# Kernel optimization log

Hardware: AMD Instinct MI355X
Metric: run time of the kernel (lower is better)

## Reference

```python
import jax, jax.numpy as jnp
import numpy as np

K_QUERY = 3    # opt.k: each point assigned to its 3 nearest SOM nodes
SOM_K = 9      # opt.som_k: 3x3 SOM neighborhood
EPS = 1e-5


def _lin1d(w, b, h):
    # 1x1 conv1d + relu: h is B,Cin,N
    return jax.nn.relu(jnp.einsum('oi,bin->bon', w, h) + b[None, :, None])


def _lin2d(w, b, h):
    # 1x1 conv2d + relu: h is B,Cin,M,K
    return jax.nn.relu(jnp.einsum('oi,bimk->bomk', w, h) + b[None, :, None, None])


def _gather_nb(feat, I):
    # feat: B,C,M ; I: B,M,K (node indices) -> B,C,M,K
    B, C, M = feat.shape
    K = I.shape[2]
    idx = jnp.broadcast_to(I[:, None, :, :], (B, C, M, K))
    return jnp.take_along_axis(feat[:, :, :, None], idx, axis=2)


def setup_inputs():
    key = jax.random.key(0)
    B, N, M = 8, 8192, 64
    ks = jax.random.split(key, 16)
    def w(k, o, i):
        return (jax.random.normal(k, (o, i), jnp.float32) / np.sqrt(i).astype(np.float32))
    return {
        'x': jax.random.normal(ks[0], (B, 3, N), jnp.float32),
        'sn': jax.random.normal(ks[1], (B, 3, N), jnp.float32),
        'node': jax.random.normal(ks[2], (B, 3, M), jnp.float32),
        'node_knn_I': jax.random.randint(ks[3], (B, M, SOM_K), 0, M),
        # PointResNet(6, [64,128,256,384])
        'pr_w0': w(ks[4], 64, 6), 'pr_b0': jnp.zeros((64,), jnp.float32),
        'pr_w1': w(ks[5], 128, 64), 'pr_b1': jnp.zeros((128,), jnp.float32),
        'pr_w2': w(ks[6], 256, 128), 'pr_b2': jnp.zeros((256,), jnp.float32),
        'pr_w3': w(ks[7], 384, 64 + 256), 'pr_b3': jnp.zeros((384,), jnp.float32),
        # KNNModule(3+384, (512,512))
        'knn_w0': w(ks[8], 512, 3 + 384), 'knn_b0': jnp.zeros((512,), jnp.float32),
        'knn_w1': w(ks[9], 512, 512), 'knn_b1': jnp.zeros((512,), jnp.float32),
        # final PointNet(3+512, (768,1024))
        'fin_w0': w(ks[10], 768, 3 + 512), 'fin_b0': jnp.zeros((768,), jnp.float32),
        'fin_w1': w(ks[11], 1024, 768), 'fin_b1': jnp.zeros((1024,), jnp.float32),
    }


def reference(x, sn, node, node_knn_I, pr_w0, pr_b0, pr_w1, pr_b1, pr_w2, pr_b2,
              pr_w3, pr_b3, knn_w0, knn_b0, knn_w1, knn_b1, fin_w0, fin_b0,
              fin_w1, fin_b1):
    B, _, N = x.shape
    M = node.shape[2]
    k = K_QUERY
    kN = k * N
    # --- som.query_topk: assign each point to its k nearest SOM nodes ---
    xd = jax.lax.stop_gradient(x)
    dist = jnp.sum((node[:, :, :, None] - xd[:, :, None, :]) ** 2, axis=1)  # B,M,N
    _, idx = jax.lax.top_k(-jnp.swapaxes(dist, 1, 2), k)                     # B,N,k
    min_idx = jnp.transpose(idx, (0, 2, 1)).reshape(B, kN)                   # B,kN (k blocks of N)
    mask = jax.nn.one_hot(min_idx, M, dtype=x.dtype)                         # B,kN,M
    mask_row_sum = jnp.sum(mask, axis=1)                                     # B,M
    mask_row_max = jnp.max(mask, axis=1) > 0                                 # B,M
    x_stack = jnp.tile(x, (1, 1, k))                                         # B,3,kN
    sn_stack = jnp.tile(sn, (1, 1, k))
    # --- masked segment-mean -> per-node cluster centers (detached) ---
    cluster_mean = jax.lax.stop_gradient(
        jnp.einsum('bcn,bnm->bcm', x_stack, mask) / (mask_row_sum[:, None, :] + EPS))
    centers = jnp.einsum('bcm,bnm->bcn', cluster_mean, mask)                 # B,3,kN
    x_decentered = jax.lax.stop_gradient(x_stack - centers)
    x_aug = jnp.concatenate([x_decentered, sn_stack], axis=1)                # B,6,kN
    # --- PointResNet(6,[64,128,256,384]) ---
    h0 = _lin1d(pr_w0, pr_b0, x_aug)
    h1 = _lin1d(pr_w1, pr_b1, h0)
    h2 = _lin1d(pr_w2, pr_b2, h1)
    first = _lin1d(pr_w3, pr_b3, jnp.concatenate([h0, h2], axis=1))          # B,384,kN
    # --- index_max scatter-max: per-node per-channel max over assigned points ---
    seg = (min_idx + (jnp.arange(B)[:, None] * M)).reshape(-1)               # (B*kN,)
    data = jnp.transpose(first, (0, 2, 1)).reshape(B * kN, -1)               # (B*kN, C)
    node_max = jax.ops.segment_max(data, seg, num_segments=B * M)            # (B*M, C)
    node_max = jnp.transpose(node_max.reshape(B, M, -1), (0, 2, 1))          # B,C,M
    # empty nodes gather index 0 in the original (gather_index * mask_row_max)
    first_masked_max = jnp.where(mask_row_max[:, None, :], node_max, first[:, :, 0:1])
    # --- KNNModule over SOM nodes (som_k=9, 'avg' centering) ---
    coord_knn = _gather_nb(cluster_mean, node_knn_I)                         # B,3,M,K
    center = jnp.mean(coord_knn, axis=3)                                     # B,3,M
    feat_knn = _gather_nb(first_masked_max, node_knn_I)                      # B,384,M,K
    aug = jnp.concatenate([coord_knn - center[:, :, :, None], feat_knn], axis=1)
    g = _lin2d(knn_w1, knn_b1, _lin2d(knn_w0, knn_b0, aug))                  # B,512,M,K
    knn_feature = jnp.max(g, axis=3)                                         # B,512,M
    # --- final PointNet(3+512,(768,1024)) + global max pool ---
    f = _lin1d(fin_w1, fin_b1,
               _lin1d(fin_w0, fin_b0, jnp.concatenate([center, knn_feature], axis=1)))
    return jnp.max(f, axis=2)                                                # B,1024
```

## Files before the change

kernel.cpp:

```cpp
#include <hip/hip_runtime.h>

typedef unsigned short u16;
typedef unsigned int   u32;
typedef _Float16 f16;
typedef _Float16 f16x8 __attribute__((ext_vector_type(8)));
typedef _Float16 f16x4 __attribute__((ext_vector_type(4)));
typedef float    f32x4 __attribute__((ext_vector_type(4)));

#define BQ 8
#define NQ 8192
#define MQ 64
#define SEGS (BQ*MQ)
#define MAXCHUNK 3584
#define KBA 10
#define NCOLS_D 4608

#define OFF_IDX      (size_t)0
#define OFF_PERM     (size_t)786432
#define OFF_CNT      (size_t)1572864
#define OFF_SUMS     (size_t)1574912
#define OFF_OFFS     (size_t)1581056
#define OFF_CURSOR   (size_t)1583360
#define OFF_NCHUNK   (size_t)1585408
#define OFF_CHUNKTAB (size_t)1585664
#define OFF_MEAN     (size_t)1614336
#define OFF_FALLBACK (size_t)1620480
#define OFF_NODEMAX  (size_t)1632768
#define OFF_CENTER   (size_t)2419200
#define OFF_W1P      (size_t)2425344
#define OFF_W2P      (size_t)2441728
#define OFF_W3P      (size_t)2507264
#define OFF_KNW0P    (size_t)2753024
#define OFF_KNW1P    (size_t)3179008
#define OFF_FINW0P   (size_t)3703296
#define OFF_FINW1P   (size_t)4538880
#define OFF_AUG      (size_t)6111744
#define OFF_MID1     (size_t)9945600
#define OFF_GBUF     (size_t)14664192
#define OFF_KEIN     (size_t)19382784
#define OFF_MIDE     (size_t)19939840

__device__ __forceinline__ void wpack(const float* __restrict__ W, f16* __restrict__ out,
                                      int K, int KB, int NF, int idx) {
  int e  = idx & 7;
  int l  = (idx >> 3) & 63;
  int kb = (idx >> 9) % KB;
  int rt = idx / (KB << 9);
  int row = rt * 16 + (l & 15);
  int c = kb * 32 + ((l >> 4) << 3) + e;
  int oc;
  if (NF < 0) oc = (c < K) ? c : -1;
  else        oc = (c < NF) ? (3 + c) : ((c < NF + 3) ? (c - NF) : -1);
  out[idx] = (oc >= 0) ? (f16)W[row * K + oc] : (f16)0.f;
}
__global__ __launch_bounds__(256) void kW(
    const float* pr_w1, const float* pr_w2, const float* pr_w3,
    const float* knn_w0, const float* knn_w1, const float* fin_w0, const float* fin_w1,
    f16* w1p, f16* w2p, f16* w3p, f16* knw0p, f16* knw1p, f16* finw0p, f16* finw1p) {
  int blk = blockIdx.x;
  int t = threadIdx.x;
  if (blk < 32)        wpack(pr_w1,  w1p,   64,  2, -1, blk * 256 + t);
  else if (blk < 160)  wpack(pr_w2,  w2p,  128,  4, -1, (blk - 32) * 256 + t);
  else if (blk < 640)  wpack(pr_w3,  w3p,  320, 10, -1, (blk - 160) * 256 + t);
  else if (blk < 1472) wpack(knn_w0, knw0p, 387, 13, 384, (blk - 640) * 256 + t);
  else if (blk < 2496) wpack(knn_w1, knw1p, 512, 16, -1, (blk - 1472) * 256 + t);
  else if (blk < 4128) wpack(fin_w0, finw0p, 515, 17, 512, (blk - 2496) * 256 + t);
  else                 wpack(fin_w1, finw1p, 768, 24, -1, (blk - 4128) * 256 + t);
}

__global__ __launch_bounds__(256) void kA(const float* __restrict__ x, const float* __restrict__ node,
                                          int* __restrict__ idx_buf, int* __restrict__ cnt,
                                          float* __restrict__ sums) {
#pragma clang fp contract(off)
  __shared__ float ns[3][64];
  __shared__ int cbin[64];
  __shared__ float sbin[3][64];
  int b = blockIdx.y;
  int t = threadIdx.x;
  if (t < 192) { int c = t >> 6, m = t & 63; ns[c][m] = node[(b * 3 + c) * 64 + m]; }
  if (t < 64) { cbin[t] = 0; sbin[0][t] = 0.f; sbin[1][t] = 0.f; sbin[2][t] = 0.f; }
  __syncthreads();
  int n = blockIdx.x * 256 + t;
  float x0 = x[(b * 3 + 0) * NQ + n];
  float x1 = x[(b * 3 + 1) * NQ + n];
  float x2 = x[(b * 3 + 2) * NQ + n];
  float d0 = 3.4e38f, d1 = 3.4e38f, d2 = 3.4e38f;
  int i0 = 0, i1 = 0, i2 = 0;
  for (int m = 0; m < 64; ++m) {
    float da = ns[0][m] - x0;
    float db = ns[1][m] - x1;
    float dc = ns[2][m] - x2;
    float d = da * da + db * db + dc * dc;
    if (d < d0)      { d2 = d1; i2 = i1; d1 = d0; i1 = i0; d0 = d; i0 = m; }
    else if (d < d1) { d2 = d1; i2 = i1; d1 = d;  i1 = m; }
    else if (d < d2) { d2 = d;  i2 = m; }
  }
  int base = (b * NQ + n) * 3;
  idx_buf[base + 0] = i0; idx_buf[base + 1] = i1; idx_buf[base + 2] = i2;
  int ms[3] = {i0, i1, i2};
  #pragma unroll
  for (int j = 0; j < 3; ++j) {
    int m = ms[j];
    atomicAdd(&cbin[m], 1);
    atomicAdd(&sbin[0][m], x0);
    atomicAdd(&sbin[1][m], x1);
    atomicAdd(&sbin[2][m], x2);
  }
  __syncthreads();
  if (t < 64 && cbin[t] > 0) {
    atomicAdd(&cnt[b * 64 + t], cbin[t]);
    atomicAdd(&sums[(b * 64 + t) * 3 + 0], sbin[0][t]);
    atomicAdd(&sums[(b * 64 + t) * 3 + 1], sbin[1][t]);
    atomicAdd(&sums[(b * 64 + t) * 3 + 2], sbin[2][t]);
  }
}

__global__ __launch_bounds__(256) void kB(const int* __restrict__ cnt, const float* __restrict__ sums,
                                          int* __restrict__ offs, int* __restrict__ cursor,
                                          int* __restrict__ nchunks, int* __restrict__ chunk_tab,
                                          float* __restrict__ mean) {
  __shared__ int sps[256], spc[256];
  int t = threadIdx.x;
  int c0 = cnt[2 * t], c1 = cnt[2 * t + 1];
  sps[t] = c0 + c1;
  spc[t] = ((c0 + 63) >> 6) + ((c1 + 63) >> 6);
  __syncthreads();
  for (int d = 1; d < 256; d <<= 1) {
    int a = 0, q = 0;
    if (t >= d) { a = sps[t - d]; q = spc[t - d]; }
    __syncthreads();
    if (t >= d) { sps[t] += a; spc[t] += q; }
    __syncthreads();
  }
  int pbase = t ? sps[t - 1] : 0;
  int cbase = t ? spc[t - 1] : 0;
  offs[2 * t] = pbase;        offs[2 * t + 1] = pbase + c0;
  cursor[2 * t] = pbase;      cursor[2 * t + 1] = pbase + c0;
  if (t == 255) { offs[512] = sps[255]; nchunks[0] = spc[255]; }
  int st = pbase, ci = cbase, s = 2 * t, c = c0;
  #pragma unroll
  for (int rep = 0; rep < 2; ++rep) {
    while (c > 0) {
      int l = c > 64 ? 64 : c;
      chunk_tab[2 * ci] = (s << 16) | l;
      chunk_tab[2 * ci + 1] = st;
      st += l; c -= l; ++ci;
    }
    s = 2 * t + 1; c = c1; st = pbase + c0;
  }
  for (int i = t; i < SEGS * 3; i += 256) mean[i] = sums[i] / ((float)cnt[i / 3] + 1e-5f);
}

__global__ __launch_bounds__(256) void kA2(const int* __restrict__ idx_buf, int* __restrict__ cursor,
                                           int* __restrict__ perm) {
  int b = blockIdx.y;
  int n = blockIdx.x * 256 + threadIdx.x;
  int base = (b * NQ + n) * 3;
  #pragma unroll
  for (int j = 0; j < 3; ++j) {
    int m = idx_buf[base + j];
    int pos = atomicAdd(&cursor[b * 64 + m], 1);
    perm[pos] = (b << 21) | (n << 8) | (j << 6) | m;
  }
}

__global__ __launch_bounds__(256) void kCtr(const float* __restrict__ mean,
                                            const int* __restrict__ knn_I,
                                            float* __restrict__ centerb) {
  int seg = blockIdx.x * 256 + threadIdx.x;
  if (seg >= SEGS) return;
  int b = seg >> 6;
  float s0 = 0, s1 = 0, s2 = 0;
  for (int kk = 0; kk < 9; ++kk) {
    int nb = knn_I[seg * 9 + kk];
    s0 += mean[(b * 64 + nb) * 3 + 0];
    s1 += mean[(b * 64 + nb) * 3 + 1];
    s2 += mean[(b * 64 + nb) * 3 + 2];
  }
  centerb[seg * 3 + 0] = s0 * (1.f / 9.f);
  centerb[seg * 3 + 1] = s1 * (1.f / 9.f);
  centerb[seg * 3 + 2] = s2 * (1.f / 9.f);
}

__global__ __launch_bounds__(512) void kC(
    const float* __restrict__ x, const float* __restrict__ sn,
    const float* __restrict__ mean, const int* __restrict__ perm,
    const int* __restrict__ chunk_tab, const int* __restrict__ nchunks,
    const float* __restrict__ w0, const float* __restrict__ b0v,
    const f16* __restrict__ w1p, const float* __restrict__ b1v,
    const f16* __restrict__ w2p, const float* __restrict__ b2v,
    const f16* __restrict__ w3p, const float* __restrict__ b3v,
    float* __restrict__ node_max, float* __restrict__ fallback) {
  __shared__ __align__(16) f16 bufA[4 * KBA * 64 * 8];
  __shared__ __align__(16) f16 bufH1[4 * 4 * 64 * 8];
  __shared__ float in_s[6][64];
  __shared__ int flag_s[64];
  int blk = blockIdx.x;
  if (blk >= nchunks[0]) return;
  int e0    = chunk_tab[2 * blk];
  int start = chunk_tab[2 * blk + 1];
  int seg = e0 >> 16, len = e0 & 0xffff;
  int b = seg >> 6;
  int tid = threadIdx.x;
  if (tid < 64) {
    float v0 = 0, v1 = 0, v2 = 0, v3 = 0, v4 = 0, v5 = 0;
    int fl = 0;
    if (tid < len) {
      int rec = perm[start + tid];
      int n = (rec >> 8) & 0x1fff;
      int j = (rec >> 6) & 3;
      const float* xb = x  + (size_t)b * 3 * NQ;
      const float* sb = sn + (size_t)b * 3 * NQ;
      v0 = xb[n]          - mean[seg * 3 + 0];
      v1 = xb[NQ + n]     - mean[seg * 3 + 1];
      v2 = xb[2 * NQ + n] - mean[seg * 3 + 2];
      v3 = sb[n]; v4 = sb[NQ + n]; v5 = sb[2 * NQ + n];
      fl = (n == 0 && j == 0) ? 1 : 0;
    }
    in_s[0][tid] = v0; in_s[1][tid] = v1; in_s[2][tid] = v2;
    in_s[3][tid] = v3; in_s[4][tid] = v4; in_s[5][tid] = v5;
    flag_s[tid] = fl;
  }
  __syncthreads();
  int wid  = __builtin_amdgcn_readfirstlane(tid >> 6);
  int lane = tid & 63;
  int pcol = lane & 15;
  int g    = lane >> 4;

  {
    float a0 = in_s[0][lane], a1 = in_s[1][lane], a2 = in_s[2][lane];
    float a3 = in_s[3][lane], a4 = in_s[4][lane], a5 = in_s[5][lane];
    f16x8 v;
    #pragma unroll
    for (int i = 0; i < 8; ++i) {
      const float* wr = w0 + (wid * 8 + i) * 6;
      float s = b0v[wid * 8 + i];
      s = fmaf(wr[0], a0, s); s = fmaf(wr[1], a1, s); s = fmaf(wr[2], a2, s);
      s = fmaf(wr[3], a3, s); s = fmaf(wr[4], a4, s); s = fmaf(wr[5], a5, s);
      v[i] = (f16)fmaxf(s, 0.f);
    }
    int kb = wid >> 2, q = wid & 3;
    *(f16x8*)&bufA[(((lane >> 4) * KBA + kb) * 64 + pcol + 16 * q) * 8] = v;
  }
  __syncthreads();

  f32x4 acc1[4] = {};
  #pragma unroll
  for (int kb = 0; kb < 2; ++kb) {
    f16x8 af = *(const f16x8*)(w1p + (size_t)((wid * 2 + kb) * 64 + lane) * 8);
    #pragma unroll
    for (int pt = 0; pt < 4; ++pt) {
      f16x8 bf = *(const f16x8*)&bufA[((pt * KBA + kb) * 64 + lane) * 8];
      acc1[pt] = __builtin_amdgcn_mfma_f32_16x16x32_f16(af, bf, acc1[pt], 0, 0, 0);
    }
  }
  {
    float4 bb = *(const float4*)&b1v[wid * 16 + g * 4];
    int kbo = wid >> 1;
    int q   = ((wid & 1) << 1) + (g >> 1);
    int ee  = (g & 1) * 4;
    #pragma unroll
    for (int pt = 0; pt < 4; ++pt) {
      f16x4 v;
      v[0] = (f16)fmaxf(acc1[pt][0] + bb.x, 0.f);
      v[1] = (f16)fmaxf(acc1[pt][1] + bb.y, 0.f);
      v[2] = (f16)fmaxf(acc1[pt][2] + bb.z, 0.f);
      v[3] = (f16)fmaxf(acc1[pt][3] + bb.w, 0.f);
      *(f16x4*)&bufH1[((pt * 4 + kbo) * 64 + pcol + 16 * q) * 8 + ee] = v;
    }
  }
  __syncthreads();

  f32x4 acc2[2][4] = {};
  #pragma unroll
  for (int kb = 0; kb < 4; ++kb) {
    f16x8 af0 = *(const f16x8*)(w2p + (size_t)(((wid * 2 + 0) * 4 + kb) * 64 + lane) * 8);
    f16x8 af1 = *(const f16x8*)(w2p + (size_t)(((wid * 2 + 1) * 4 + kb) * 64 + lane) * 8);
    #pragma unroll
    for (int pt = 0; pt < 4; ++pt) {
      f16x8 bf = *(const f16x8*)&bufH1[((pt * 4 + kb) * 64 + lane) * 8];
      acc2[0][pt] = __builtin_amdgcn_mfma_f32_16x16x32_f16(af0, bf, acc2[0][pt], 0, 0, 0);
      acc2[1][pt] = __builtin_amdgcn_mfma_f32_16x16x32_f16(af1, bf, acc2[1][pt], 0, 0, 0);
    }
  }
  {
    int kbo = 2 + wid;
    #pragma unroll
    for (int s = 0; s < 2; ++s) {
      float4 bb = *(const float4*)&b2v[(wid * 2 + s) * 16 + g * 4];
      int q  = 2 * s + (g >> 1);
      int ee = (g & 1) * 4;
      #pragma unroll
      for (int pt = 0; pt < 4; ++pt) {
        f16x4 v;
        v[0] = (f16)fmaxf(acc2[s][pt][0] + bb.x, 0.f);
        v[1] = (f16)fmaxf(acc2[s][pt][1] + bb.y, 0.f);
        v[2] = (f16)fmaxf(acc2[s][pt][2] + bb.z, 0.f);
        v[3] = (f16)fmaxf(acc2[s][pt][3] + bb.w, 0.f);
        *(f16x4*)&bufA[((pt * KBA + kbo) * 64 + pcol + 16 * q) * 8 + ee] = v;
      }
    }
  }
  __syncthreads();

  f32x4 acc3[3][4] = {};
  #pragma unroll
  for (int kb = 0; kb < KBA; ++kb) {
    f16x8 af0 = *(const f16x8*)(w3p + (size_t)(((wid * 3 + 0) * KBA + kb) * 64 + lane) * 8);
    f16x8 af1 = *(const f16x8*)(w3p + (size_t)(((wid * 3 + 1) * KBA + kb) * 64 + lane) * 8);
    f16x8 af2 = *(const f16x8*)(w3p + (size_t)(((wid * 3 + 2) * KBA + kb) * 64 + lane) * 8);
    #pragma unroll
    for (int pt = 0; pt < 4; ++pt) {
      f16x8 bf = *(const f16x8*)&bufA[((pt * KBA + kb) * 64 + lane) * 8];
      acc3[0][pt] = __builtin_amdgcn_mfma_f32_16x16x32_f16(af0, bf, acc3[0][pt], 0, 0, 0);
      acc3[1][pt] = __builtin_amdgcn_mfma_f32_16x16x32_f16(af1, bf, acc3[1][pt], 0, 0, 0);
      acc3[2][pt] = __builtin_amdgcn_mfma_f32_16x16x32_f16(af2, bf, acc3[2][pt], 0, 0, 0);
    }
  }
  {
    int fl[4], vld[4];
    #pragma unroll
    for (int pt = 0; pt < 4; ++pt) {
      fl[pt]  = flag_s[pt * 16 + pcol];
      vld[pt] = (pt * 16 + pcol) < len;
    }
    #pragma unroll
    for (int c = 0; c < 3; ++c) {
      int ct = wid * 3 + c;
      float4 bb = *(const float4*)&b3v[ct * 16 + g * 4];
      float bj[4] = {bb.x, bb.y, bb.z, bb.w};
      #pragma unroll
      for (int j = 0; j < 4; ++j) {
        float vm = 0.f;
        #pragma unroll
        for (int pt = 0; pt < 4; ++pt) {
          float v = fmaxf(acc3[c][pt][j] + bj[j], 0.f);
          if (fl[pt]) fallback[b * 384 + ct * 16 + g * 4 + j] = v;
          if (!vld[pt]) v = 0.f;
          vm = fmaxf(vm, v);
        }
        vm = fmaxf(vm, __shfl_xor(vm, 1));
        vm = fmaxf(vm, __shfl_xor(vm, 2));
        vm = fmaxf(vm, __shfl_xor(vm, 4));
        vm = fmaxf(vm, __shfl_xor(vm, 8));
        if (pcol == 0)
          atomicMax((int*)&node_max[(size_t)seg * 384 + ct * 16 + g * 4 + j],
                    __float_as_int(vm));
      }
    }
  }
}

__global__ __launch_bounds__(256) void kDg(
    const float* __restrict__ mean, const float* __restrict__ node_max,
    const float* __restrict__ fallback, const int* __restrict__ cnt,
    const int* __restrict__ knn_I, const float* __restrict__ centerb,
    f16* __restrict__ augP) {
  int idx = blockIdx.x * 256 + threadIdx.x;
  if (idx < NCOLS_D * 48) {
    int col = idx / 48;
    int rg  = idx - col * 48;
    int kk = col >> 9, seg = col & 511, b = seg >> 6;
    int nb = knn_I[seg * 9 + kk];
    const float* src = (cnt[b * 64 + nb] > 0) ? (node_max + (size_t)(b * 64 + nb) * 384)
                                              : (fallback + (size_t)b * 384);
    int r = rg * 8;
    f16x8 v;
    #pragma unroll
    for (int e = 0; e < 8; ++e) v[e] = (f16)src[r + e];
    int ct = col >> 4, pc = col & 15;
    int kb = r >> 5, ks = (r >> 3) & 3;
    *(f16x8*)&augP[(size_t)((ct * 13 + kb) * 64 + pc + 16 * ks) * 8] = v;
  } else if (idx < NCOLS_D * 48 + NCOLS_D) {
    int col = idx - NCOLS_D * 48;
    int kk = col >> 9, seg = col & 511, b = seg >> 6;
    int nb = knn_I[seg * 9 + kk];
    f16x8 v = {};
    #pragma unroll
    for (int c = 0; c < 3; ++c)
      v[c] = (f16)(mean[(b * 64 + nb) * 3 + c] - centerb[seg * 3 + c]);
    int ct = col >> 4, pc = col & 15;
    *(f16x8*)&augP[(size_t)((ct * 13 + 12) * 64 + pc) * 8] = v;
    f16x8 z = {};
    #pragma unroll
    for (int ks = 1; ks < 4; ++ks)
      *(f16x8*)&augP[(size_t)((ct * 13 + 12) * 64 + pc + 16 * ks) * 8] = z;
  }
}

template<int NKB_IN, int NKB_OUT, int MODE>
__global__ __launch_bounds__(256) void kGemm(
    const f16* __restrict__ Ap, const f16* __restrict__ Bp,
    const float* __restrict__ bias, f16* __restrict__ outP, float* __restrict__ outF) {
  int cb = blockIdx.x;
  int rb = blockIdx.y;
  int tid = threadIdx.x;
  int wid = __builtin_amdgcn_readfirstlane(tid >> 6);
  int lane = tid & 63;
  int rt = rb * 4 + wid;
  f32x4 acc[4] = {};
  const f16* ap = Ap + (size_t)rt * NKB_IN * 512;
  const f16* bp = Bp + (size_t)cb * 4 * NKB_IN * 512;
  #pragma unroll
  for (int kb = 0; kb < NKB_IN; ++kb) {
    f16x8 af = *(const f16x8*)(ap + (size_t)(kb * 64 + lane) * 8);
    #pragma unroll
    for (int ct = 0; ct < 4; ++ct) {
      f16x8 bf = *(const f16x8*)(bp + (size_t)((ct * NKB_IN + kb) * 64 + lane) * 8);
      acc[ct] = __builtin_amdgcn_mfma_f32_16x16x32_f16(af, bf, acc[ct], 0, 0, 0);
    }
  }
  int pcol = lane & 15, g = lane >> 4;
  float4 bb = *(const float4*)&bias[rt * 16 + g * 4];
  float bj[4] = {bb.x, bb.y, bb.z, bb.w};
  if (MODE == 0) {
    int k0 = rt * 16 + g * 4;
    int kb2 = k0 >> 5, ks2 = (k0 >> 3) & 3, ee = k0 & 7;
    #pragma unroll
    for (int ct = 0; ct < 4; ++ct) {
      f16x4 v;
      #pragma unroll
      for (int j = 0; j < 4; ++j) v[j] = (f16)fmaxf(acc[ct][j] + bj[j], 0.f);
      int ctc = cb * 4 + ct;
      *(f16x4*)&outP[(size_t)((ctc * NKB_OUT + kb2) * 64 + pcol + 16 * ks2) * 8 + ee] = v;
    }
  } else if (MODE == 1) {
    #pragma unroll
    for (int ct = 0; ct < 4; ++ct) {
      f16x4 v;
      #pragma unroll
      for (int j = 0; j < 4; ++j) v[j] = (f16)fmaxf(acc[ct][j] + bj[j], 0.f);
      int col = cb * 64 + ct * 16 + pcol;
      *(f16x4*)&outP[(size_t)col * 512 + rt * 16 + g * 4] = v;
    }
  } else {
    #pragma unroll
    for (int j = 0; j < 4; ++j) {
      float v = fmaxf(acc[0][j] + bj[j], 0.f);
      #pragma unroll
      for (int ct = 1; ct < 4; ++ct) v = fmaxf(v, fmaxf(acc[ct][j] + bj[j], 0.f));
      v = fmaxf(v, __shfl_xor(v, 1));
      v = fmaxf(v, __shfl_xor(v, 2));
      v = fmaxf(v, __shfl_xor(v, 4));
      v = fmaxf(v, __shfl_xor(v, 8));
      if (pcol == 0) outF[cb * 1024 + rt * 16 + g * 4 + j] = v;
    }
  }
}

__global__ __launch_bounds__(256) void kDmax(const f16* __restrict__ gbuf,
                                             const float* __restrict__ centerb,
                                             f16* __restrict__ keinP) {
  int idx = blockIdx.x * 256 + threadIdx.x;
  if (idx < SEGS * 64) {
    int seg = idx >> 6;
    int rg  = idx & 63;
    int r = rg * 8;
    float m[8] = {};
    for (int kk = 0; kk < 9; ++kk) {
      f16x8 gv = *(const f16x8*)&gbuf[(size_t)(kk * 512 + seg) * 512 + r];
      #pragma unroll
      for (int e = 0; e < 8; ++e) m[e] = fmaxf(m[e], (float)gv[e]);
    }
    f16x8 v;
    #pragma unroll
    for (int e = 0; e < 8; ++e) v[e] = (f16)m[e];
    int ct = seg >> 4, pc = seg & 15;
    int kb = r >> 5, ks = (r >> 3) & 3;
    *(f16x8*)&keinP[(size_t)((ct * 17 + kb) * 64 + pc + 16 * ks) * 8] = v;
  } else if (idx < SEGS * 64 + SEGS) {
    int seg = idx - SEGS * 64;
    f16x8 v = {};
    #pragma unroll
    for (int c = 0; c < 3; ++c) v[c] = (f16)centerb[seg * 3 + c];
    int ct = seg >> 4, pc = seg & 15;
    *(f16x8*)&keinP[(size_t)((ct * 17 + 16) * 64 + pc) * 8] = v;
    f16x8 z = {};
    #pragma unroll
    for (int ks = 1; ks < 4; ++ks)
      *(f16x8*)&keinP[(size_t)((ct * 17 + 16) * 64 + pc + 16 * ks) * 8] = z;
  }
}

extern "C" void kernel_launch(void* const* d_in, const int* in_sizes, int n_in,
                              void* d_out, int out_size, void* d_ws, size_t ws_size,
                              hipStream_t stream) {
  const float* x      = (const float*)d_in[0];
  const float* sn     = (const float*)d_in[1];
  const float* node   = (const float*)d_in[2];
  const int*   knn_I  = (const int*)d_in[3];
  const float* pr_w0  = (const float*)d_in[4];
  const float* pr_b0  = (const float*)d_in[5];
  const float* pr_w1  = (const float*)d_in[6];
  const float* pr_b1  = (const float*)d_in[7];
  const float* pr_w2  = (const float*)d_in[8];
  const float* pr_b2  = (const float*)d_in[9];
  const float* pr_w3  = (const float*)d_in[10];
  const float* pr_b3  = (const float*)d_in[11];
  const float* knn_w0 = (const float*)d_in[12];
  const float* knn_b0 = (const float*)d_in[13];
  const float* knn_w1 = (const float*)d_in[14];
  const float* knn_b1 = (const float*)d_in[15];
  const float* fin_w0 = (const float*)d_in[16];
  const float* fin_b0 = (const float*)d_in[17];
  const float* fin_w1 = (const float*)d_in[18];
  const float* fin_b1 = (const float*)d_in[19];
  float* out = (float*)d_out;
  char* ws = (char*)d_ws;

  int*   idx_buf   = (int*)(ws + OFF_IDX);
  int*   perm      = (int*)(ws + OFF_PERM);
  int*   cnt       = (int*)(ws + OFF_CNT);
  float* sums      = (float*)(ws + OFF_SUMS);
  int*   offs      = (int*)(ws + OFF_OFFS);
  int*   cursor    = (int*)(ws + OFF_CURSOR);
  int*   nchunks   = (int*)(ws + OFF_NCHUNK);
  int*   chunk_tab = (int*)(ws + OFF_CHUNKTAB);
  float* mean      = (float*)(ws + OFF_MEAN);
  float* fallback  = (float*)(ws + OFF_FALLBACK);
  float* node_max  = (float*)(ws + OFF_NODEMAX);
  float* centerb   = (float*)(ws + OFF_CENTER);
  f16*   w1p       = (f16*)(ws + OFF_W1P);
  f16*   w2p       = (f16*)(ws + OFF_W2P);
  f16*   w3p       = (f16*)(ws + OFF_W3P);
  f16*   knw0p     = (f16*)(ws + OFF_KNW0P);
  f16*   knw1p     = (f16*)(ws + OFF_KNW1P);
  f16*   finw0p    = (f16*)(ws + OFF_FINW0P);
  f16*   finw1p    = (f16*)(ws + OFF_FINW1P);
  f16*   augP      = (f16*)(ws + OFF_AUG);
  f16*   mid1P     = (f16*)(ws + OFF_MID1);
  f16*   gbuf      = (f16*)(ws + OFF_GBUF);
  f16*   keinP     = (f16*)(ws + OFF_KEIN);
  f16*   midEP     = (f16*)(ws + OFF_MIDE);

  hipMemsetAsync(ws + OFF_CNT, 0, 8192, stream);
  hipMemsetAsync(ws + OFF_NODEMAX, 0, (size_t)SEGS * 384 * 4, stream);

  kW<<<7200, 256, 0, stream>>>(pr_w1, pr_w2, pr_w3, knn_w0, knn_w1, fin_w0, fin_w1,
                               w1p, w2p, w3p, knw0p, knw1p, finw0p, finw1p);

  dim3 gA(NQ / 256, BQ);
  kA<<<gA, 256, 0, stream>>>(x, node, idx_buf, cnt, sums);
  kB<<<1, 256, 0, stream>>>(cnt, sums, offs, cursor, nchunks, chunk_tab, mean);
  kA2<<<gA, 256, 0, stream>>>(idx_buf, cursor, perm);
  kCtr<<<2, 256, 0, stream>>>(mean, knn_I, centerb);
  kC<<<MAXCHUNK, 512, 0, stream>>>(x, sn, mean, perm, chunk_tab, nchunks,
                                   pr_w0, pr_b0, w1p, pr_b1, w2p, pr_b2, w3p, pr_b3,
                                   node_max, fallback);
  kDg<<<(NCOLS_D * 48 + NCOLS_D + 255) / 256, 256, 0, stream>>>(
      mean, node_max, fallback, cnt, knn_I, centerb, augP);
  kGemm<13, 16, 0><<<dim3(72, 8), 256, 0, stream>>>(knw0p, augP, knn_b0, mid1P, nullptr);
  kGemm<16, 0, 1><<<dim3(72, 8), 256, 0, stream>>>(knw1p, mid1P, knn_b1, gbuf, nullptr);
  kDmax<<<(SEGS * 64 + SEGS + 255) / 256, 256, 0, stream>>>(gbuf, centerb, keinP);
  kGemm<17, 24, 0><<<dim3(8, 12), 256, 0, stream>>>(finw0p, keinP, fin_b0, midEP, nullptr);
  kGemm<24, 0, 2><<<dim3(8, 16), 256, 0, stream>>>(finw1p, midEP, fin_b1, nullptr, out);
}
```

Baseline: 291.1 us.

## Make point-MLP kernel persistent with register-resident weights, padded LDS, fused center

```diff
diff --git a/kernel.cpp b/kernel.cpp
--- a/kernel.cpp
+++ b/kernel.cpp
@@ -14,6 +14,7 @@
 #define MAXCHUNK 3584
 #define KBA 10
 #define NCOLS_D 4608
+#define ROWL 520
 
 #define OFF_IDX      (size_t)0
 #define OFF_PERM     (size_t)786432
@@ -118,7 +119,8 @@
 __global__ __launch_bounds__(256) void kB(const int* __restrict__ cnt, const float* __restrict__ sums,
                                           int* __restrict__ offs, int* __restrict__ cursor,
                                           int* __restrict__ nchunks, int* __restrict__ chunk_tab,
-                                          float* __restrict__ mean) {
+                                          float* __restrict__ mean, const int* __restrict__ knn_I,
+                                          float* __restrict__ centerb) {
   __shared__ int sps[256], spc[256];
   int t = threadIdx.x;
   int c0 = cnt[2 * t], c1 = cnt[2 * t + 1];
@@ -149,40 +151,45 @@
     s = 2 * t + 1; c = c1; st = pbase + c0;
   }
   for (int i = t; i < SEGS * 3; i += 256) mean[i] = sums[i] / ((float)cnt[i / 3] + 1e-5f);
+  for (int seg = t; seg < SEGS; seg += 256) {
+    int b = seg >> 6;
+    float s0 = 0.f, s1 = 0.f, s2 = 0.f;
+    for (int kk = 0; kk < 9; ++kk) {
+      int q = b * 64 + knn_I[seg * 9 + kk];
+      float inv = 1.f / ((float)cnt[q] + 1e-5f);
+      s0 += sums[q * 3 + 0] * inv;
+      s1 += sums[q * 3 + 1] * inv;
+      s2 += sums[q * 3 + 2] * inv;
+    }
+    centerb[seg * 3 + 0] = s0 * (1.f / 9.f);
+    centerb[seg * 3 + 1] = s1 * (1.f / 9.f);
+    centerb[seg * 3 + 2] = s2 * (1.f / 9.f);
+  }
 }
 
 __global__ __launch_bounds__(256) void kA2(const int* __restrict__ idx_buf, int* __restrict__ cursor,
                                            int* __restrict__ perm) {
+  __shared__ int loc[64];
+  __shared__ int base_s[64];
   int b = blockIdx.y;
-  int n = blockIdx.x * 256 + threadIdx.x;
+  int t = threadIdx.x;
+  if (t < 64) loc[t] = 0;
+  __syncthreads();
+  int n = blockIdx.x * 256 + t;
   int base = (b * NQ + n) * 3;
-  #pragma unroll
-  for (int j = 0; j < 3; ++j) {
-    int m = idx_buf[base + j];
-    int pos = atomicAdd(&cursor[b * 64 + m], 1);
-    perm[pos] = (b << 21) | (n << 8) | (j << 6) | m;
-  }
-}
-
-__global__ __launch_bounds__(256) void kCtr(const float* __restrict__ mean,
-                                            const int* __restrict__ knn_I,
-                                            float* __restrict__ centerb) {
-  int seg = blockIdx.x * 256 + threadIdx.x;
-  if (seg >= SEGS) return;
-  int b = seg >> 6;
-  float s0 = 0, s1 = 0, s2 = 0;
-  for (int kk = 0; kk < 9; ++kk) {
-    int nb = knn_I[seg * 9 + kk];
-    s0 += mean[(b * 64 + nb) * 3 + 0];
-    s1 += mean[(b * 64 + nb) * 3 + 1];
-    s2 += mean[(b * 64 + nb) * 3 + 2];
-  }
-  centerb[seg * 3 + 0] = s0 * (1.f / 9.f);
-  centerb[seg * 3 + 1] = s1 * (1.f / 9.f);
-  centerb[seg * 3 + 2] = s2 * (1.f / 9.f);
-}
-
-__global__ __launch_bounds__(512) void kC(
+  int m0 = idx_buf[base + 0], m1 = idx_buf[base + 1], m2 = idx_buf[base + 2];
+  int l0 = atomicAdd(&loc[m0], 1);
+  int l1 = atomicAdd(&loc[m1], 1);
+  int l2 = atomicAdd(&loc[m2], 1);
+  __syncthreads();
+  if (t < 64 && loc[t] > 0) base_s[t] = atomicAdd(&cursor[b * 64 + t], loc[t]);
+  __syncthreads();
+  perm[base_s[m0] + l0] = (b << 21) | (n << 8) | (0 << 6) | m0;
+  perm[base_s[m1] + l1] = (b << 21) | (n << 8) | (1 << 6) | m1;
+  perm[base_s[m2] + l2] = (b << 21) | (n << 8) | (2 << 6) | m2;
+}
+
+__global__ __launch_bounds__(512, 2) void kC(
     const float* __restrict__ x, const float* __restrict__ sn,
     const float* __restrict__ mean, const int* __restrict__ perm,
     const int* __restrict__ chunk_tab, const int* __restrict__ nchunks,
@@ -191,161 +198,182 @@
     const f16* __restrict__ w2p, const float* __restrict__ b2v,
     const f16* __restrict__ w3p, const float* __restrict__ b3v,
     float* __restrict__ node_max, float* __restrict__ fallback) {
-  __shared__ __align__(16) f16 bufA[4 * KBA * 64 * 8];
-  __shared__ __align__(16) f16 bufH1[4 * 4 * 64 * 8];
+  __shared__ __align__(16) f16 bufA[4 * KBA * ROWL];
+  __shared__ __align__(16) f16 bufH1[4 * 4 * ROWL];
   __shared__ float in_s[6][64];
+  __shared__ float w0_s[448];
+  __shared__ float b3_s[384];
   __shared__ int flag_s[64];
-  int blk = blockIdx.x;
-  if (blk >= nchunks[0]) return;
-  int e0    = chunk_tab[2 * blk];
-  int start = chunk_tab[2 * blk + 1];
-  int seg = e0 >> 16, len = e0 & 0xffff;
-  int b = seg >> 6;
+  __shared__ int n_s[64];
   int tid = threadIdx.x;
-  if (tid < 64) {
-    float v0 = 0, v1 = 0, v2 = 0, v3 = 0, v4 = 0, v5 = 0;
-    int fl = 0;
-    if (tid < len) {
-      int rec = perm[start + tid];
-      int n = (rec >> 8) & 0x1fff;
-      int j = (rec >> 6) & 3;
-      const float* xb = x  + (size_t)b * 3 * NQ;
-      const float* sb = sn + (size_t)b * 3 * NQ;
-      v0 = xb[n]          - mean[seg * 3 + 0];
-      v1 = xb[NQ + n]     - mean[seg * 3 + 1];
-      v2 = xb[2 * NQ + n] - mean[seg * 3 + 2];
-      v3 = sb[n]; v4 = sb[NQ + n]; v5 = sb[2 * NQ + n];
-      fl = (n == 0 && j == 0) ? 1 : 0;
-    }
-    in_s[0][tid] = v0; in_s[1][tid] = v1; in_s[2][tid] = v2;
-    in_s[3][tid] = v3; in_s[4][tid] = v4; in_s[5][tid] = v5;
-    flag_s[tid] = fl;
-  }
-  __syncthreads();
   int wid  = __builtin_amdgcn_readfirstlane(tid >> 6);
   int lane = tid & 63;
   int pcol = lane & 15;
   int g    = lane >> 4;
 
-  {
-    float a0 = in_s[0][lane], a1 = in_s[1][lane], a2 = in_s[2][lane];
-    float a3 = in_s[3][lane], a4 = in_s[4][lane], a5 = in_s[5][lane];
-    f16x8 v;
-    #pragma unroll
-    for (int i = 0; i < 8; ++i) {
-      const float* wr = w0 + (wid * 8 + i) * 6;
-      float s = b0v[wid * 8 + i];
-      s = fmaf(wr[0], a0, s); s = fmaf(wr[1], a1, s); s = fmaf(wr[2], a2, s);
-      s = fmaf(wr[3], a3, s); s = fmaf(wr[4], a4, s); s = fmaf(wr[5], a5, s);
-      v[i] = (f16)fmaxf(s, 0.f);
-    }
-    int kb = wid >> 2, q = wid & 3;
-    *(f16x8*)&bufA[(((lane >> 4) * KBA + kb) * 64 + pcol + 16 * q) * 8] = v;
-  }
-  __syncthreads();
-
-  f32x4 acc1[4] = {};
+  for (int i = tid; i < 384; i += 512) { w0_s[i] = w0[i]; b3_s[i] = b3v[i]; }
+  if (tid < 64) w0_s[384 + tid] = b0v[tid];
+
+  f16x8 af2h[2];
   #pragma unroll
-  for (int kb = 0; kb < 2; ++kb) {
-    f16x8 af = *(const f16x8*)(w1p + (size_t)((wid * 2 + kb) * 64 + lane) * 8);
-    #pragma unroll
-    for (int pt = 0; pt < 4; ++pt) {
-      f16x8 bf = *(const f16x8*)&bufA[((pt * KBA + kb) * 64 + lane) * 8];
-      acc1[pt] = __builtin_amdgcn_mfma_f32_16x16x32_f16(af, bf, acc1[pt], 0, 0, 0);
-    }
-  }
-  {
-    float4 bb = *(const float4*)&b1v[wid * 16 + g * 4];
-    int kbo = wid >> 1;
-    int q   = ((wid & 1) << 1) + (g >> 1);
-    int ee  = (g & 1) * 4;
-    #pragma unroll
-    for (int pt = 0; pt < 4; ++pt) {
-      f16x4 v;
-      v[0] = (f16)fmaxf(acc1[pt][0] + bb.x, 0.f);
-      v[1] = (f16)fmaxf(acc1[pt][1] + bb.y, 0.f);
-      v[2] = (f16)fmaxf(acc1[pt][2] + bb.z, 0.f);
-      v[3] = (f16)fmaxf(acc1[pt][3] + bb.w, 0.f);
-      *(f16x4*)&bufH1[((pt * 4 + kbo) * 64 + pcol + 16 * q) * 8 + ee] = v;
-    }
-  }
-  __syncthreads();
-
-  f32x4 acc2[2][4] = {};
+  for (int kb = 0; kb < 2; ++kb)
+    af2h[kb] = *(const f16x8*)(w1p + (size_t)((wid * 2 + kb) * 64 + lane) * 8);
+  f16x8 af4h[3][KBA];
   #pragma unroll
-  for (int kb = 0; kb < 4; ++kb) {
-    f16x8 af0 = *(const f16x8*)(w2p + (size_t)(((wid * 2 + 0) * 4 + kb) * 64 + lane) * 8);
-    f16x8 af1 = *(const f16x8*)(w2p + (size_t)(((wid * 2 + 1) * 4 + kb) * 64 + lane) * 8);
-    #pragma unroll
-    for (int pt = 0; pt < 4; ++pt) {
-      f16x8 bf = *(const f16x8*)&bufH1[((pt * 4 + kb) * 64 + lane) * 8];
-      acc2[0][pt] = __builtin_amdgcn_mfma_f32_16x16x32_f16(af0, bf, acc2[0][pt], 0, 0, 0);
-      acc2[1][pt] = __builtin_amdgcn_mfma_f32_16x16x32_f16(af1, bf, acc2[1][pt], 0, 0, 0);
-    }
-  }
-  {
-    int kbo = 2 + wid;
-    #pragma unroll
-    for (int s = 0; s < 2; ++s) {
-      float4 bb = *(const float4*)&b2v[(wid * 2 + s) * 16 + g * 4];
-      int q  = 2 * s + (g >> 1);
-      int ee = (g & 1) * 4;
+  for (int c = 0; c < 3; ++c)
+    #pragma unroll
+    for (int kb = 0; kb < KBA; ++kb)
+      af4h[c][kb] = *(const f16x8*)(w3p + (size_t)(((wid * 3 + c) * KBA + kb) * 64 + lane) * 8);
+
+  int nch = nchunks[0];
+  for (int blk = blockIdx.x; blk < nch; blk += gridDim.x) {
+    __syncthreads();
+    int e0    = chunk_tab[2 * blk];
+    int start = chunk_tab[2 * blk + 1];
+    int seg = e0 >> 16, len = e0 & 0xffff;
+    int b = seg >> 6;
+    if (tid < 64) {
+      int n = 0, fl = 0;
+      if (tid < len) {
+        int rec = perm[start + tid];
+        n = (rec >> 8) & 0x1fff;
+        fl = (n == 0 && (((rec >> 6) & 3) == 0)) ? 1 : 0;
+      }
+      n_s[tid] = n;
+      flag_s[tid] = fl;
+    }
+    __syncthreads();
+    {
+      int p = tid >> 3, c = tid & 7;
+      if (c < 6) {
+        int n = n_s[p];
+        float v;
+        if (c < 3) v = x[((size_t)b * 3 + c) * NQ + n] - mean[seg * 3 + c];
+        else       v = sn[((size_t)b * 3 + (c - 3)) * NQ + n];
+        in_s[c][p] = v;
+      }
+    }
+    f16x8 af3[2][4];
+    #pragma unroll
+    for (int s = 0; s < 2; ++s)
+      #pragma unroll
+      for (int kb = 0; kb < 4; ++kb)
+        af3[s][kb] = *(const f16x8*)(w2p + (size_t)(((wid * 2 + s) * 4 + kb) * 64 + lane) * 8);
+    __syncthreads();
+
+    {
+      float a0 = in_s[0][lane], a1 = in_s[1][lane], a2 = in_s[2][lane];
+      float a3 = in_s[3][lane], a4 = in_s[4][lane], a5 = in_s[5][lane];
+      f16x8 v;
+      #pragma unroll
+      for (int i = 0; i < 8; ++i) {
+        const float* wr = &w0_s[(wid * 8 + i) * 6];
+        float s = w0_s[384 + wid * 8 + i];
+        s = fmaf(wr[0], a0, s); s = fmaf(wr[1], a1, s); s = fmaf(wr[2], a2, s);
+        s = fmaf(wr[3], a3, s); s = fmaf(wr[4], a4, s); s = fmaf(wr[5], a5, s);
+        v[i] = (f16)fmaxf(s, 0.f);
+      }
+      int kb = wid >> 2, q = wid & 3;
+      *(f16x8*)&bufA[(g * KBA + kb) * ROWL + (pcol + 16 * q) * 8] = v;
+    }
+    __syncthreads();
+
+    f32x4 acc1[4] = {};
+    #pragma unroll
+    for (int kb = 0; kb < 2; ++kb) {
+      #pragma unroll
+      for (int pt = 0; pt < 4; ++pt) {
+        f16x8 bf = *(const f16x8*)&bufA[(pt * KBA + kb) * ROWL + lane * 8];
+        acc1[pt] = __builtin_amdgcn_mfma_f32_16x16x32_f16(af2h[kb], bf, acc1[pt], 0, 0, 0);
+      }
+    }
+    {
+      float4 bb = *(const float4*)&b1v[wid * 16 + g * 4];
+      int kbo = wid >> 1;
+      int q   = ((wid & 1) << 1) + (g >> 1);
+      int ee  = (g & 1) * 4;
       #pragma unroll
       for (int pt = 0; pt < 4; ++pt) {
         f16x4 v;
-        v[0] = (f16)fmaxf(acc2[s][pt][0] + bb.x, 0.f);
-        v[1] = (f16)fmaxf(acc2[s][pt][1] + bb.y, 0.f);
-        v[2] = (f16)fmaxf(acc2[s][pt][2] + bb.z, 0.f);
-        v[3] = (f16)fmaxf(acc2[s][pt][3] + bb.w, 0.f);
-        *(f16x4*)&bufA[((pt * KBA + kbo) * 64 + pcol + 16 * q) * 8 + ee] = v;
-      }
-    }
-  }
-  __syncthreads();
-
-  f32x4 acc3[3][4] = {};
-  #pragma unroll
-  for (int kb = 0; kb < KBA; ++kb) {
-    f16x8 af0 = *(const f16x8*)(w3p + (size_t)(((wid * 3 + 0) * KBA + kb) * 64 + lane) * 8);
-    f16x8 af1 = *(const f16x8*)(w3p + (size_t)(((wid * 3 + 1) * KBA + kb) * 64 + lane) * 8);
-    f16x8 af2 = *(const f16x8*)(w3p + (size_t)(((wid * 3 + 2) * KBA + kb) * 64 + lane) * 8);
-    #pragma unroll
-    for (int pt = 0; pt < 4; ++pt) {
-      f16x8 bf = *(const f16x8*)&bufA[((pt * KBA + kb) * 64 + lane) * 8];
-      acc3[0][pt] = __builtin_amdgcn_mfma_f32_16x16x32_f16(af0, bf, acc3[0][pt], 0, 0, 0);
-      acc3[1][pt] = __builtin_amdgcn_mfma_f32_16x16x32_f16(af1, bf, acc3[1][pt], 0, 0, 0);
-      acc3[2][pt] = __builtin_amdgcn_mfma_f32_16x16x32_f16(af2, bf, acc3[2][pt], 0, 0, 0);
-    }
-  }
-  {
-    int fl[4], vld[4];
-    #pragma unroll
-    for (int pt = 0; pt < 4; ++pt) {
-      fl[pt]  = flag_s[pt * 16 + pcol];
-      vld[pt] = (pt * 16 + pcol) < len;
-    }
-    #pragma unroll
-    for (int c = 0; c < 3; ++c) {
-      int ct = wid * 3 + c;
-      float4 bb = *(const float4*)&b3v[ct * 16 + g * 4];
-      float bj[4] = {bb.x, bb.y, bb.z, bb.w};
-      #pragma unroll
-      for (int j = 0; j < 4; ++j) {
-        float vm = 0.f;
+        v[0] = (f16)fmaxf(acc1[pt][0] + bb.x, 0.f);
+        v[1] = (f16)fmaxf(acc1[pt][1] + bb.y, 0.f);
+        v[2] = (f16)fmaxf(acc1[pt][2] + bb.z, 0.f);
+        v[3] = (f16)fmaxf(acc1[pt][3] + bb.w, 0.f);
+        *(f16x4*)&bufH1[(pt * 4 + kbo) * ROWL + (pcol + 16 * q) * 8 + ee] = v;
+      }
+    }
+    __syncthreads();
+
+    f32x4 acc2[2][4] = {};
+    #pragma unroll
+    for (int kb = 0; kb < 4; ++kb) {
+      #pragma unroll
+      for (int pt = 0; pt < 4; ++pt) {
+        f16x8 bf = *(const f16x8*)&bufH1[(pt * 4 + kb) * ROWL + lane * 8];
+        acc2[0][pt] = __builtin_amdgcn_mfma_f32_16x16x32_f16(af3[0][kb], bf, acc2[0][pt], 0, 0, 0);
+        acc2[1][pt] = __builtin_amdgcn_mfma_f32_16x16x32_f16(af3[1][kb], bf, acc2[1][pt], 0, 0, 0);
+      }
+    }
+    {
+      int kbo = 2 + wid;
+      #pragma unroll
+      for (int s = 0; s < 2; ++s) {
+        float4 bb = *(const float4*)&b2v[(wid * 2 + s) * 16 + g * 4];
+        int q  = 2 * s + (g >> 1);
+        int ee = (g & 1) * 4;
         #pragma unroll
         for (int pt = 0; pt < 4; ++pt) {
-          float v = fmaxf(acc3[c][pt][j] + bj[j], 0.f);
-          if (fl[pt]) fallback[b * 384 + ct * 16 + g * 4 + j] = v;
-          if (!vld[pt]) v = 0.f;
-          vm = fmaxf(vm, v);
+          f16x4 v;
+          v[0] = (f16)fmaxf(acc2[s][pt][0] + bb.x, 0.f);
+          v[1] = (f16)fmaxf(acc2[s][pt][1] + bb.y, 0.f);
+          v[2] = (f16)fmaxf(acc2[s][pt][2] + bb.z, 0.f);
+          v[3] = (f16)fmaxf(acc2[s][pt][3] + bb.w, 0.f);
+          *(f16x4*)&bufA[(pt * KBA + kbo) * ROWL + (pcol + 16 * q) * 8 + ee] = v;
         }
-        vm = fmaxf(vm, __shfl_xor(vm, 1));
-        vm = fmaxf(vm, __shfl_xor(vm, 2));
-        vm = fmaxf(vm, __shfl_xor(vm, 4));
-        vm = fmaxf(vm, __shfl_xor(vm, 8));
-        if (pcol == 0)
-          atomicMax((int*)&node_max[(size_t)seg * 384 + ct * 16 + g * 4 + j],
-                    __float_as_int(vm));
+      }
+    }
+    __syncthreads();
+
+    f32x4 acc3[3][4] = {};
+    #pragma unroll
+    for (int kb = 0; kb < KBA; ++kb) {
+      #pragma unroll
+      for (int pt = 0; pt < 4; ++pt) {
+        f16x8 bf = *(const f16x8*)&bufA[(pt * KBA + kb) * ROWL + lane * 8];
+        acc3[0][pt] = __builtin_amdgcn_mfma_f32_16x16x32_f16(af4h[0][kb], bf, acc3[0][pt], 0, 0, 0);
+        acc3[1][pt] = __builtin_amdgcn_mfma_f32_16x16x32_f16(af4h[1][kb], bf, acc3[1][pt], 0, 0, 0);
+        acc3[2][pt] = __builtin_amdgcn_mfma_f32_16x16x32_f16(af4h[2][kb], bf, acc3[2][pt], 0, 0, 0);
+      }
+    }
+    {
+      int fl[4], vld[4];
+      #pragma unroll
+      for (int pt = 0; pt < 4; ++pt) {
+        fl[pt]  = flag_s[pt * 16 + pcol];
+        vld[pt] = (pt * 16 + pcol) < len;
+      }
+      #pragma unroll
+      for (int c = 0; c < 3; ++c) {
+        int ct = wid * 3 + c;
+        #pragma unroll
+        for (int j = 0; j < 4; ++j) {
+          float bj = b3_s[ct * 16 + g * 4 + j];
+          float vm = 0.f;
+          #pragma unroll
+          for (int pt = 0; pt < 4; ++pt) {
+            float v = fmaxf(acc3[c][pt][j] + bj, 0.f);
+            if (fl[pt]) fallback[b * 384 + ct * 16 + g * 4 + j] = v;
+            if (!vld[pt]) v = 0.f;
+            vm = fmaxf(vm, v);
+          }
+          vm = fmaxf(vm, __shfl_xor(vm, 1));
+          vm = fmaxf(vm, __shfl_xor(vm, 2));
+          vm = fmaxf(vm, __shfl_xor(vm, 4));
+          vm = fmaxf(vm, __shfl_xor(vm, 8));
+          if (pcol == 0)
+            atomicMax((int*)&node_max[(size_t)seg * 384 + ct * 16 + g * 4 + j],
+                      __float_as_int(vm));
+        }
       }
     }
   }
@@ -541,12 +569,11 @@
 
   dim3 gA(NQ / 256, BQ);
   kA<<<gA, 256, 0, stream>>>(x, node, idx_buf, cnt, sums);
-  kB<<<1, 256, 0, stream>>>(cnt, sums, offs, cursor, nchunks, chunk_tab, mean);
+  kB<<<1, 256, 0, stream>>>(cnt, sums, offs, cursor, nchunks, chunk_tab, mean, knn_I, centerb);
   kA2<<<gA, 256, 0, stream>>>(idx_buf, cursor, perm);
-  kCtr<<<2, 256, 0, stream>>>(mean, knn_I, centerb);
-  kC<<<MAXCHUNK, 512, 0, stream>>>(x, sn, mean, perm, chunk_tab, nchunks,
-                                   pr_w0, pr_b0, w1p, pr_b1, w2p, pr_b2, w3p, pr_b3,
-                                   node_max, fallback);
+  kC<<<256, 512, 0, stream>>>(x, sn, mean, perm, chunk_tab, nchunks,
+                              pr_w0, pr_b0, w1p, pr_b1, w2p, pr_b2, w3p, pr_b3,
+                              node_max, fallback);
   kDg<<<(NCOLS_D * 48 + NCOLS_D + 255) / 256, 256, 0, stream>>>(
       mean, node_max, fallback, cnt, knn_I, centerb, augP);
   kGemm<13, 16, 0><<<dim3(72, 8), 256, 0, stream>>>(knw0p, augP, knn_b0, mid1P, nullptr);
```

New measurement: 287.4 us. No clear change (-1.3%).

## Fuse center computation into scan kernel and aggregate scatter atomics in LDS

Applied to the files above, without the earlier changes.

```diff
diff --git a/kernel.cpp b/kernel.cpp
--- a/kernel.cpp
+++ b/kernel.cpp
@@ -118,7 +118,8 @@
 __global__ __launch_bounds__(256) void kB(const int* __restrict__ cnt, const float* __restrict__ sums,
                                           int* __restrict__ offs, int* __restrict__ cursor,
                                           int* __restrict__ nchunks, int* __restrict__ chunk_tab,
-                                          float* __restrict__ mean) {
+                                          float* __restrict__ mean, const int* __restrict__ knn_I,
+                                          float* __restrict__ centerb, f16* __restrict__ keinP) {
   __shared__ int sps[256], spc[256];
   int t = threadIdx.x;
   int c0 = cnt[2 * t], c1 = cnt[2 * t + 1];
@@ -149,37 +150,51 @@
     s = 2 * t + 1; c = c1; st = pbase + c0;
   }
   for (int i = t; i < SEGS * 3; i += 256) mean[i] = sums[i] / ((float)cnt[i / 3] + 1e-5f);
+  for (int seg = t; seg < SEGS; seg += 256) {
+    int b = seg >> 6;
+    float s0 = 0.f, s1 = 0.f, s2 = 0.f;
+    for (int kk = 0; kk < 9; ++kk) {
+      int q = b * 64 + knn_I[seg * 9 + kk];
+      float inv = 1.f / ((float)cnt[q] + 1e-5f);
+      s0 += sums[q * 3 + 0] * inv;
+      s1 += sums[q * 3 + 1] * inv;
+      s2 += sums[q * 3 + 2] * inv;
+    }
+    s0 *= (1.f / 9.f); s1 *= (1.f / 9.f); s2 *= (1.f / 9.f);
+    centerb[seg * 3 + 0] = s0;
+    centerb[seg * 3 + 1] = s1;
+    centerb[seg * 3 + 2] = s2;
+    int ct = seg >> 4, pc = seg & 15;
+    f16x8 cv = {};
+    cv[0] = (f16)s0; cv[1] = (f16)s1; cv[2] = (f16)s2;
+    *(f16x8*)&keinP[(size_t)((ct * 17 + 16) * 64 + pc) * 8] = cv;
+    f16x8 z = {};
+    #pragma unroll
+    for (int ks = 1; ks < 4; ++ks)
+      *(f16x8*)&keinP[(size_t)((ct * 17 + 16) * 64 + pc + 16 * ks) * 8] = z;
+  }
 }
 
 __global__ __launch_bounds__(256) void kA2(const int* __restrict__ idx_buf, int* __restrict__ cursor,
                                            int* __restrict__ perm) {
+  __shared__ int loc[64];
+  __shared__ int base_s[64];
   int b = blockIdx.y;
-  int n = blockIdx.x * 256 + threadIdx.x;
+  int t = threadIdx.x;
+  if (t < 64) loc[t] = 0;
+  __syncthreads();
+  int n = blockIdx.x * 256 + t;
   int base = (b * NQ + n) * 3;
-  #pragma unroll
-  for (int j = 0; j < 3; ++j) {
-    int m = idx_buf[base + j];
-    int pos = atomicAdd(&cursor[b * 64 + m], 1);
-    perm[pos] = (b << 21) | (n << 8) | (j << 6) | m;
-  }
-}
-
-__global__ __launch_bounds__(256) void kCtr(const float* __restrict__ mean,
-                                            const int* __restrict__ knn_I,
-                                            float* __restrict__ centerb) {
-  int seg = blockIdx.x * 256 + threadIdx.x;
-  if (seg >= SEGS) return;
-  int b = seg >> 6;
-  float s0 = 0, s1 = 0, s2 = 0;
-  for (int kk = 0; kk < 9; ++kk) {
-    int nb = knn_I[seg * 9 + kk];
-    s0 += mean[(b * 64 + nb) * 3 + 0];
-    s1 += mean[(b * 64 + nb) * 3 + 1];
-    s2 += mean[(b * 64 + nb) * 3 + 2];
-  }
-  centerb[seg * 3 + 0] = s0 * (1.f / 9.f);
-  centerb[seg * 3 + 1] = s1 * (1.f / 9.f);
-  centerb[seg * 3 + 2] = s2 * (1.f / 9.f);
+  int m0 = idx_buf[base + 0], m1 = idx_buf[base + 1], m2 = idx_buf[base + 2];
+  int l0 = atomicAdd(&loc[m0], 1);
+  int l1 = atomicAdd(&loc[m1], 1);
+  int l2 = atomicAdd(&loc[m2], 1);
+  __syncthreads();
+  if (t < 64 && loc[t] > 0) base_s[t] = atomicAdd(&cursor[b * 64 + t], loc[t]);
+  __syncthreads();
+  perm[base_s[m0] + l0] = (b << 21) | (n << 8) | (0 << 6) | m0;
+  perm[base_s[m1] + l1] = (b << 21) | (n << 8) | (1 << 6) | m1;
+  perm[base_s[m2] + l2] = (b << 21) | (n << 8) | (2 << 6) | m2;
 }
 
 __global__ __launch_bounds__(512) void kC(
@@ -389,7 +404,7 @@
 }
 
 template<int NKB_IN, int NKB_OUT, int MODE>
-__global__ __launch_bounds__(256) void kGemm(
+__global__ __launch_bounds__(256, 1) void kGemm(
     const f16* __restrict__ Ap, const f16* __restrict__ Bp,
     const float* __restrict__ bias, f16* __restrict__ outP, float* __restrict__ outF) {
   int cb = blockIdx.x;
@@ -449,37 +464,24 @@
 }
 
 __global__ __launch_bounds__(256) void kDmax(const f16* __restrict__ gbuf,
-                                             const float* __restrict__ centerb,
                                              f16* __restrict__ keinP) {
   int idx = blockIdx.x * 256 + threadIdx.x;
-  if (idx < SEGS * 64) {
-    int seg = idx >> 6;
-    int rg  = idx & 63;
-    int r = rg * 8;
-    float m[8] = {};
-    for (int kk = 0; kk < 9; ++kk) {
-      f16x8 gv = *(const f16x8*)&gbuf[(size_t)(kk * 512 + seg) * 512 + r];
-      #pragma unroll
-      for (int e = 0; e < 8; ++e) m[e] = fmaxf(m[e], (float)gv[e]);
-    }
-    f16x8 v;
-    #pragma unroll
-    for (int e = 0; e < 8; ++e) v[e] = (f16)m[e];
-    int ct = seg >> 4, pc = seg & 15;
-    int kb = r >> 5, ks = (r >> 3) & 3;
-    *(f16x8*)&keinP[(size_t)((ct * 17 + kb) * 64 + pc + 16 * ks) * 8] = v;
-  } else if (idx < SEGS * 64 + SEGS) {
-    int seg = idx - SEGS * 64;
-    f16x8 v = {};
-    #pragma unroll
-    for (int c = 0; c < 3; ++c) v[c] = (f16)centerb[seg * 3 + c];
-    int ct = seg >> 4, pc = seg & 15;
-    *(f16x8*)&keinP[(size_t)((ct * 17 + 16) * 64 + pc) * 8] = v;
-    f16x8 z = {};
-    #pragma unroll
-    for (int ks = 1; ks < 4; ++ks)
-      *(f16x8*)&keinP[(size_t)((ct * 17 + 16) * 64 + pc + 16 * ks) * 8] = z;
-  }
+  if (idx >= SEGS * 64) return;
+  int seg = idx >> 6;
+  int rg  = idx & 63;
+  int r = rg * 8;
+  float m[8] = {};
+  for (int kk = 0; kk < 9; ++kk) {
+    f16x8 gv = *(const f16x8*)&gbuf[(size_t)(kk * 512 + seg) * 512 + r];
+    #pragma unroll
+    for (int e = 0; e < 8; ++e) m[e] = fmaxf(m[e], (float)gv[e]);
+  }
+  f16x8 v;
+  #pragma unroll
+  for (int e = 0; e < 8; ++e) v[e] = (f16)m[e];
+  int ct = seg >> 4, pc = seg & 15;
+  int kb = r >> 5, ks = (r >> 3) & 3;
+  *(f16x8*)&keinP[(size_t)((ct * 17 + kb) * 64 + pc + 16 * ks) * 8] = v;
 }
 
 extern "C" void kernel_launch(void* const* d_in, const int* in_sizes, int n_in,
@@ -541,9 +543,9 @@
 
   dim3 gA(NQ / 256, BQ);
   kA<<<gA, 256, 0, stream>>>(x, node, idx_buf, cnt, sums);
-  kB<<<1, 256, 0, stream>>>(cnt, sums, offs, cursor, nchunks, chunk_tab, mean);
+  kB<<<1, 256, 0, stream>>>(cnt, sums, offs, cursor, nchunks, chunk_tab, mean, knn_I,
+                            centerb, keinP);
   kA2<<<gA, 256, 0, stream>>>(idx_buf, cursor, perm);
-  kCtr<<<2, 256, 0, stream>>>(mean, knn_I, centerb);
   kC<<<MAXCHUNK, 512, 0, stream>>>(x, sn, mean, perm, chunk_tab, nchunks,
                                    pr_w0, pr_b0, w1p, pr_b1, w2p, pr_b2, w3p, pr_b3,
                                    node_max, fallback);
@@ -551,7 +553,7 @@
       mean, node_max, fallback, cnt, knn_I, centerb, augP);
   kGemm<13, 16, 0><<<dim3(72, 8), 256, 0, stream>>>(knw0p, augP, knn_b0, mid1P, nullptr);
   kGemm<16, 0, 1><<<dim3(72, 8), 256, 0, stream>>>(knw1p, mid1P, knn_b1, gbuf, nullptr);
-  kDmax<<<(SEGS * 64 + SEGS + 255) / 256, 256, 0, stream>>>(gbuf, centerb, keinP);
+  kDmax<<<SEGS * 64 / 256, 256, 0, stream>>>(gbuf, keinP);
   kGemm<17, 24, 0><<<dim3(8, 12), 256, 0, stream>>>(finw0p, keinP, fin_b0, midEP, nullptr);
   kGemm<24, 0, 2><<<dim3(8, 16), 256, 0, stream>>>(finw1p, midEP, fin_b1, nullptr, out);
 }
```

After: 249.6 us. 14.3% less time.
